# Kernel optimization log

Measured on AMD Instinct MI355X. Metric: run time of the kernel, lower is better.

## Reference

```python
import jax, jax.numpy as jnp
import numpy as np

D_MODEL = 2048
NUM_HEADS = 16
HEAD_DIM = D_MODEL // NUM_HEADS
SCALE = 1.0 / np.sqrt(HEAD_DIM).astype(np.float32)
NEG_INF = -1e9


def setup_inputs() -> dict:
    key = jax.random.key(0)
    ks = jax.random.split(key, 10)
    B, S = 2, 2048
    x = jax.random.normal(ks[0], (B, S, D_MODEL), dtype=jnp.float32)
    # causal lower-triangular mask, broadcastable over (B, H)
    causal_mask = jnp.tril(jnp.ones((S, S), dtype=jnp.int32))[None, None]
    init = 1.0 / np.sqrt(D_MODEL)
    def lin(kw, kb):
        W = jax.random.uniform(kw, (D_MODEL, D_MODEL), jnp.float32, -init, init)
        b = jax.random.uniform(kb, (D_MODEL,), jnp.float32, -init, init)
        return W, b
    Wq, bq = lin(ks[1], ks[2])
    Wk, bk = lin(ks[3], ks[4])
    Wv, bv = lin(ks[5], ks[6])
    Wo, bo = lin(ks[7], ks[8])
    return {"x": x, "causal_mask": causal_mask,
            "Wq": Wq, "bq": bq, "Wk": Wk, "bk": bk,
            "Wv": Wv, "bv": bv, "Wo": Wo, "bo": bo}


def reference(x, causal_mask, Wq, bq, Wk, bk, Wv, bv, Wo, bo):
    B, S, _ = x.shape
    def proj(W, b):
        # torch Linear: x @ W.T + b -> (B, H, S, Dh)
        y = jnp.einsum('bsd,ed->bse', x, W) + b
        return y.reshape(B, S, NUM_HEADS, HEAD_DIM).transpose(0, 2, 1, 3)
    q = proj(Wq, bq)
    k = proj(Wk, bk)
    v = proj(Wv, bv)
    # apply_rope is a no-op stub in the source; q, k unchanged.
    scores = jnp.einsum('bhqd,bhkd->bhqk', q, k) * SCALE
    scores = jnp.where(causal_mask == 0, NEG_INF, scores)
    attn = jax.nn.softmax(scores, axis=-1)
    out = jnp.einsum('bhqk,bhkd->bhqd', attn, v)
    out = out.transpose(0, 2, 1, 3).reshape(B, S, D_MODEL)
    return jnp.einsum('bsd,ed->bse', out, Wo) + bo
```

## Files before the change

kernel.cpp:

```cpp
#include <hip/hip_runtime.h>
#include <hip/hip_bf16.h>
#include <stdint.h>
#include <stddef.h>

typedef __bf16 bf16_t;
typedef __bf16 bf16x4_t __attribute__((ext_vector_type(4)));
typedef __bf16 bf16x8_t __attribute__((ext_vector_type(8)));
typedef float f32x4 __attribute__((ext_vector_type(4)));

#define D_MODEL 2048
#define NHEADS 16
#define HDIM 128
#define SEQ 2048
#define BATCH 2
#define MTOT (BATCH * SEQ)
#define SCALE_F 0.08838834764831845f
#define LOG2E 1.4426950408889634f
#define QSCALE (SCALE_F * LOG2E)
#define KT 64
#define NEGI -3.0e38f
#define MINIT -1.0e30f
#define DEFER_THR 8.0f

#define AS1 __attribute__((address_space(1)))
#define AS3 __attribute__((address_space(3)))

__device__ __forceinline__ void load_lds16(const bf16_t* g, bf16_t* l) {
  __builtin_amdgcn_global_load_lds((AS1 void*)(g), (AS3 void*)(l), 16, 0, 0);
}

__global__ void cast_all_kernel(const float* __restrict__ x,
                                const float* __restrict__ w0, const float* __restrict__ w1,
                                const float* __restrict__ w2, const float* __restrict__ w3,
                                bf16_t* __restrict__ xb, bf16_t* __restrict__ wcat) {
  int i = blockIdx.x * blockDim.x + threadIdx.x;
  const int XN4 = MTOT * D_MODEL / 4;
  const int WN4 = D_MODEL * D_MODEL / 4;
  const float* src;
  bf16_t* dst;
  int idx;
  if (i < XN4) {
    src = x; dst = xb; idx = i;
  } else {
    int j = i - XN4;
    int y = j >> 20;
    idx = j & (WN4 - 1);
    src = (y == 0) ? w0 : (y == 1) ? w1 : (y == 2) ? w2 : w3;
    dst = wcat + (size_t)y * D_MODEL * D_MODEL;
  }
  float4 v = ((const float4*)src)[idx];
  bf16x4_t o;
  o.x = (bf16_t)v.x; o.y = (bf16_t)v.y; o.z = (bf16_t)v.z; o.w = (bf16_t)v.w;
  ((bf16x4_t*)dst)[idx] = o;
}

__global__ __launch_bounds__(256) void gemm_fused(
    const bf16_t* __restrict__ A, const bf16_t* __restrict__ Bm, int mode,
    const float* __restrict__ bias0, const float* __restrict__ bias1,
    const float* __restrict__ bias2,
    bf16_t* __restrict__ Qo, bf16_t* __restrict__ Ko, bf16_t* __restrict__ Vto,
    float* __restrict__ Out) {
  const int K = 2048;
  __shared__ __align__(16) bf16_t lA[128 * 64];
  __shared__ __align__(16) bf16_t lB[128 * 64];
  const int m0 = blockIdx.x * 128;
  const int n0 = blockIdx.y * 128;
  const int t = threadIdx.x;
  const int w = t >> 6, lane = t & 63;
  const int wm = w & 1, wn = w >> 1;
  const int la = lane & 15, lb = lane >> 4;

  f32x4 acc[4][4];
  f32x4 zero = {0.f, 0.f, 0.f, 0.f};
#pragma unroll
  for (int i = 0; i < 4; i++)
#pragma unroll
    for (int j = 0; j < 4; j++) acc[i][j] = zero;

  const int row0 = t >> 3, cc = t & 7;
  const int ccs = cc ^ (row0 & 7);
  const bf16_t* gA = A + (size_t)(m0 + row0) * K + ccs * 8;
  const bf16_t* gB = Bm + (size_t)(n0 + row0) * K + ccs * 8;
  bf16_t* sA = lA + t * 8;
  bf16_t* sB = lB + t * 8;

  for (int k0 = 0; k0 < K; k0 += 64) {
    __syncthreads();
#pragma unroll
    for (int i = 0; i < 4; i++)
      load_lds16(gA + k0 + (size_t)(32 * i) * K, sA + 2048 * i);
#pragma unroll
    for (int i = 0; i < 4; i++)
      load_lds16(gB + k0 + (size_t)(32 * i) * K, sB + 2048 * i);
    __syncthreads();
#pragma unroll
    for (int ks = 0; ks < 2; ks++) {
      bf16x8_t af[4], bfr[4];
#pragma unroll
      for (int mt = 0; mt < 4; mt++) {
        int row = wm * 64 + mt * 16 + la;
        af[mt] = *(const bf16x8_t*)(lA + row * 64 + (((ks * 4 + lb) ^ (la & 7)) * 8));
      }
#pragma unroll
      for (int nt = 0; nt < 4; nt++) {
        int row = wn * 64 + nt * 16 + la;
        bfr[nt] = *(const bf16x8_t*)(lB + row * 64 + (((ks * 4 + lb) ^ (la & 7)) * 8));
      }
#pragma unroll
      for (int mt = 0; mt < 4; mt++)
#pragma unroll
        for (int nt = 0; nt < 4; nt++)
          acc[mt][nt] = __builtin_amdgcn_mfma_f32_16x16x32_bf16(af[mt], bfr[nt], acc[mt][nt], 0, 0, 0);
    }
  }

  if (mode == 0) {
#pragma unroll
    for (int mt = 0; mt < 4; mt++) {
#pragma unroll
      for (int nt = 0; nt < 4; nt++) {
        int m = m0 + wm * 64 + mt * 16 + lb * 4;
        int n = n0 + wn * 64 + nt * 16 + la;
        int b = m >> 11, s = m & 2047;
        int which = n >> 11, hd = n & 2047;
        int h = hd >> 7, d = hd & 127;
        float bv = (which == 0 ? bias0 : which == 1 ? bias1 : bias2)[hd];
        f32x4 v = acc[mt][nt];
        if (which == 2) {
          bf16_t* dst = Vto + ((size_t)(b * NHEADS + h) * HDIM + d) * SEQ + s;
          bf16x4_t pk;
          pk.x = (bf16_t)(v.x + bv); pk.y = (bf16_t)(v.y + bv);
          pk.z = (bf16_t)(v.z + bv); pk.w = (bf16_t)(v.w + bv);
          *(bf16x4_t*)dst = pk;
        } else {
          float sc = (which == 0) ? QSCALE : 1.0f;
          bf16_t* dst = (which == 0 ? Qo : Ko) + ((size_t)(b * NHEADS + h) * SEQ + s) * HDIM + d;
          dst[0]        = (bf16_t)((v.x + bv) * sc);
          dst[HDIM]     = (bf16_t)((v.y + bv) * sc);
          dst[2 * HDIM] = (bf16_t)((v.z + bv) * sc);
          dst[3 * HDIM] = (bf16_t)((v.w + bv) * sc);
        }
      }
    }
  } else {
#pragma unroll
    for (int mt = 0; mt < 4; mt++) {
#pragma unroll
      for (int nt = 0; nt < 4; nt++) {
        int m = m0 + wm * 64 + mt * 16 + lb * 4;
        int n = n0 + wn * 64 + nt * 16 + la;
        float bv = bias0[n];
        f32x4 v = acc[mt][nt];
        float* dst = Out + (size_t)m * D_MODEL + n;
        dst[0]           = v.x + bv;
        dst[D_MODEL]     = v.y + bv;
        dst[2 * D_MODEL] = v.z + bv;
        dst[3 * D_MODEL] = v.w + bv;
      }
    }
  }
}

__global__ __launch_bounds__(256, 2) void flash_attn(
    const bf16_t* __restrict__ Q, const bf16_t* __restrict__ Kg,
    const bf16_t* __restrict__ Vt, bf16_t* __restrict__ O,
    bf16_t* __restrict__ PO, float* __restrict__ ML) {
  __shared__ __align__(16) bf16_t lK[2][KT * 128];
  __shared__ __align__(16) bf16_t lV[128 * KT];
  __shared__ __align__(16) bf16_t lP[128 * 72];
  const int g = blockIdx.x;
  const int bh = g & 31, idx = g >> 5;
  const int t = threadIdx.x;
  const int w = t >> 6, lane = t & 63;
  const int la = lane & 15, lb = lane >> 4;
  const int qloc = w * 32 + la;

  const bf16_t* Qb = Q + (size_t)bh * SEQ * HDIM;
  const bf16_t* Kb = Kg + (size_t)bh * SEQ * HDIM;
  const bf16_t* Vb = Vt + (size_t)bh * HDIM * SEQ;
  const int b = bh >> 4, h = bh & 15;

  int nph, qts[2], k0s[2], k1s[2], slots[2];
  bool parts[2];
  if (idx < 8) {
    nph = 1; qts[0] = 8 + idx; k0s[0] = 0; k1s[0] = 17;
    parts[0] = true; slots[0] = (idx * 32 + bh) * 2;
  } else {
    int qtA = idx - 8;
    nph = 2;
    qts[0] = qtA; k0s[0] = 0; k1s[0] = 2 * qtA + 2; parts[0] = false; slots[0] = 0;
    qts[1] = 15 - qtA; k0s[1] = 17; k1s[1] = 32 - 2 * qtA;
    parts[1] = true; slots[1] = ((7 - qtA) * 32 + bh) * 2 + 1;
  }

  const int krow = t >> 4, kcc = t & 15;
  const int kccx = kcc ^ krow;
  const int vrow = t >> 3, vjc = t & 7;
  const int vccx = vjc ^ (vrow & 7);

  for (int ph = 0; ph < nph; ph++) {
    const int qt = qts[ph], kt0 = k0s[ph], kt1 = k1s[ph];
    const int q0 = qt * 128;

    bf16x8_t qf[2][4];
#pragma unroll
    for (int mt = 0; mt < 2; mt++)
#pragma unroll
      for (int ks = 0; ks < 4; ks++)
        qf[mt][ks] = *(const bf16x8_t*)(Qb + (size_t)(q0 + qloc + mt * 16) * HDIM + ks * 32 + lb * 8);

    f32x4 oacc[2][8];
    float mr[2] = {MINIT, MINIT}, lr[2] = {0.f, 0.f};
    f32x4 zero = {0.f, 0.f, 0.f, 0.f};
#pragma unroll
    for (int mt = 0; mt < 2; mt++)
#pragma unroll
      for (int dt = 0; dt < 8; dt++) oacc[mt][dt] = zero;

    {
      const int j0 = kt0 * KT;
#pragma unroll
      for (int i = 0; i < 4; i++)
        load_lds16(Kb + (size_t)(j0 + krow + 16 * i) * HDIM + kccx * 8,
                   lK[kt0 & 1] + (t + 256 * i) * 8);
    }

    for (int kt = kt0; kt < kt1; kt++) {
      const int j0 = kt * KT;
      const int cur = kt & 1;
      const bool pre = (kt + 1 < kt1);

      __syncthreads();

#pragma unroll
      for (int i = 0; i < 4; i++)
        load_lds16(Vb + (size_t)(vrow + 32 * i) * SEQ + j0 + vccx * 8,
                   lV + (t + 256 * i) * 8);
      if (pre) {
        const int jn = (kt + 1) * KT;
#pragma unroll
        for (int i = 0; i < 4; i++)
          load_lds16(Kb + (size_t)(jn + krow + 16 * i) * HDIM + kccx * 8,
                     lK[cur ^ 1] + (t + 256 * i) * 8);
      }

      f32x4 st[4][2];
#pragma unroll
      for (int nt = 0; nt < 4; nt++)
#pragma unroll
        for (int mt = 0; mt < 2; mt++) st[nt][mt] = zero;
      __builtin_amdgcn_s_setprio(1);
#pragma unroll
      for (int ks = 0; ks < 4; ks++) {
#pragma unroll
        for (int nt = 0; nt < 4; nt++) {
          int j = nt * 16 + la;
          int ck = (ks * 4 + lb) ^ la;
          bf16x8_t kf = *(const bf16x8_t*)(lK[cur] + j * 128 + ck * 8);
#pragma unroll
          for (int mt = 0; mt < 2; mt++)
            st[nt][mt] = __builtin_amdgcn_mfma_f32_16x16x32_bf16(kf, qf[mt][ks], st[nt][mt], 0, 0, 0);
        }
      }
      __builtin_amdgcn_s_setprio(0);

      const bool dm = (j0 + KT > q0);
#pragma unroll
      for (int mt = 0; mt < 2; mt++) {
        int qg = q0 + qloc + mt * 16;
        if (dm) {
#pragma unroll
          for (int nt = 0; nt < 4; nt++)
#pragma unroll
            for (int r = 0; r < 4; r++)
              if (j0 + nt * 16 + lb * 4 + r > qg) st[nt][mt][r] = NEGI;
        }
        float tm = NEGI;
#pragma unroll
        for (int nt = 0; nt < 4; nt++)
#pragma unroll
          for (int r = 0; r < 4; r++) tm = fmaxf(tm, st[nt][mt][r]);
        tm = fmaxf(tm, __shfl_xor(tm, 16));
        tm = fmaxf(tm, __shfl_xor(tm, 32));
        if (!__all(tm - mr[mt] <= DEFER_THR)) {
          float mnew = fmaxf(mr[mt], tm);
          float alpha = exp2f(mr[mt] - mnew);
          lr[mt] *= alpha;
#pragma unroll
          for (int dt = 0; dt < 8; dt++) oacc[mt][dt] *= alpha;
          mr[mt] = mnew;
        }
        float s = 0.f;
#pragma unroll
        for (int nt = 0; nt < 4; nt++) {
          f32x4 p;
#pragma unroll
          for (int r = 0; r < 4; r++) {
            p[r] = exp2f(st[nt][mt][r] - mr[mt]);
            s += p[r];
          }
          bf16x4_t pk;
          pk.x = (bf16_t)p[0]; pk.y = (bf16_t)p[1]; pk.z = (bf16_t)p[2]; pk.w = (bf16_t)p[3];
          *(bf16x4_t*)(lP + (qloc + mt * 16) * 72 + nt * 16 + lb * 4) = pk;
        }
        s += __shfl_xor(s, 16);
        s += __shfl_xor(s, 32);
        lr[mt] += s;
      }

      if (pre) {
        asm volatile("s_waitcnt vmcnt(4)" ::: "memory");
      } else {
        asm volatile("s_waitcnt vmcnt(0)" ::: "memory");
      }
      __builtin_amdgcn_s_barrier();

      bf16x8_t pf[2][2];
#pragma unroll
      for (int mt = 0; mt < 2; mt++)
#pragma unroll
        for (int ksv = 0; ksv < 2; ksv++)
          pf[mt][ksv] = *(const bf16x8_t*)(lP + (w * 32 + mt * 16 + la) * 72 + ksv * 32 + lb * 8);
      __builtin_amdgcn_s_setprio(1);
#pragma unroll
      for (int dt = 0; dt < 8; dt++) {
        int d = dt * 16 + la;
#pragma unroll
        for (int ksv = 0; ksv < 2; ksv++) {
          int jc = (ksv * 4 + lb) ^ (d & 7);
          bf16x8_t vf = *(const bf16x8_t*)(lV + d * 64 + jc * 8);
#pragma unroll
          for (int mt = 0; mt < 2; mt++)
            oacc[mt][dt] = __builtin_amdgcn_mfma_f32_16x16x32_bf16(vf, pf[mt][ksv], oacc[mt][dt], 0, 0, 0);
        }
      }
      __builtin_amdgcn_s_setprio(0);
    }

    if (!parts[ph]) {
#pragma unroll
      for (int mt = 0; mt < 2; mt++) {
        float inv = 1.0f / lr[mt];
        int q = q0 + qloc + mt * 16;
        bf16_t* dst = O + ((size_t)b * SEQ + q) * D_MODEL + h * HDIM + lb * 4;
#pragma unroll
        for (int dt = 0; dt < 8; dt++) {
          f32x4 v = oacc[mt][dt];
          bf16x4_t pk;
          pk.x = (bf16_t)(v[0] * inv); pk.y = (bf16_t)(v[1] * inv);
          pk.z = (bf16_t)(v[2] * inv); pk.w = (bf16_t)(v[3] * inv);
          *(bf16x4_t*)(dst + dt * 16) = pk;
        }
      }
    } else {
      const int slot = slots[ph];
      bf16_t* pob = PO + (size_t)slot * 128 * 128;
#pragma unroll
      for (int mt = 0; mt < 2; mt++) {
        int q = qloc + mt * 16;
        bf16_t* dst = pob + (size_t)q * 128 + lb * 4;
#pragma unroll
        for (int dt = 0; dt < 8; dt++) {
          f32x4 v = oacc[mt][dt];
          bf16x4_t pk;
          pk.x = (bf16_t)v[0]; pk.y = (bf16_t)v[1];
          pk.z = (bf16_t)v[2]; pk.w = (bf16_t)v[3];
          *(bf16x4_t*)(dst + dt * 16) = pk;
        }
        if (lb == 0) {
          float2 ml = make_float2(mr[mt], lr[mt]);
          *(float2*)(ML + ((size_t)slot * 128 + q) * 2) = ml;
        }
      }
    }
  }
}

__global__ void merge_kernel(const bf16_t* __restrict__ PO, const float* __restrict__ ML,
                             bf16_t* __restrict__ O) {
  const int qti = blockIdx.x >> 5, bh = blockIdx.x & 31;
  const int qt = 8 + qti;
  const int t = threadIdx.x;
  const int q = t >> 1, dh = (t & 1) * 64;
  const size_t s1 = ((size_t)(qti * 32 + bh)) * 2;
  const float* ml1 = ML + (s1 * 128 + q) * 2;
  const float* ml2 = ML + ((s1 + 1) * 128 + q) * 2;
  float m1 = ml1[0], l1 = ml1[1], m2 = ml2[0], l2 = ml2[1];
  float m = fmaxf(m1, m2);
  float w1 = exp2f(m1 - m), w2 = exp2f(m2 - m);
  float inv = 1.0f / (w1 * l1 + w2 * l2);
  w1 *= inv; w2 *= inv;
  const bf16_t* p1 = PO + (s1 * 128 + q) * 128 + dh;
  const bf16_t* p2 = PO + ((s1 + 1) * 128 + q) * 128 + dh;
  const int b = bh >> 4, h = bh & 15;
  bf16_t* dst = O + ((size_t)b * SEQ + qt * 128 + q) * D_MODEL + h * HDIM + dh;
#pragma unroll
  for (int i = 0; i < 8; i++) {
    bf16x8_t a = ((const bf16x8_t*)p1)[i];
    bf16x8_t c = ((const bf16x8_t*)p2)[i];
    bf16x8_t o;
#pragma unroll
    for (int e = 0; e < 8; e++)
      o[e] = (bf16_t)(w1 * (float)a[e] + w2 * (float)c[e]);
    ((bf16x8_t*)dst)[i] = o;
  }
}

extern "C" void kernel_launch(void* const* d_in, const int* in_sizes, int n_in,
                              void* d_out, int out_size, void* d_ws, size_t ws_size,
                              hipStream_t stream) {
  (void)in_sizes; (void)n_in; (void)out_size; (void)ws_size;
  const float* x  = (const float*)d_in[0];
  const float* Wq = (const float*)d_in[2];
  const float* bq = (const float*)d_in[3];
  const float* Wk = (const float*)d_in[4];
  const float* bk = (const float*)d_in[5];
  const float* Wv = (const float*)d_in[6];
  const float* bv = (const float*)d_in[7];
  const float* Wo = (const float*)d_in[8];
  const float* bo = (const float*)d_in[9];
  float* out = (float*)d_out;

  const size_t NBF = (size_t)MTOT * D_MODEL * sizeof(bf16_t);
  const size_t WBF = (size_t)D_MODEL * D_MODEL * sizeof(bf16_t);
  char* p = (char*)d_ws;
  bf16_t* xb   = (bf16_t*)p; p += NBF;
  bf16_t* Wcat = (bf16_t*)p; p += 4 * WBF;
  bf16_t* Qb   = (bf16_t*)p; p += NBF;
  bf16_t* Kb   = (bf16_t*)p; p += NBF;
  bf16_t* Vtb  = (bf16_t*)p; p += NBF;
  bf16_t* Wob  = Wcat + (size_t)3 * D_MODEL * D_MODEL;
  bf16_t* Ob   = xb;
  bf16_t* PO = Wcat;
  float*  ML = (float*)(Wcat + (size_t)512 * 128 * 128);

  const int XN4 = MTOT * D_MODEL / 4;
  const int WN4 = D_MODEL * D_MODEL / 4;
  cast_all_kernel<<<(XN4 + 4 * WN4) / 256, 256, 0, stream>>>(x, Wq, Wk, Wv, Wo, xb, Wcat);

  gemm_fused<<<dim3(MTOT / 128, 6144 / 128), 256, 0, stream>>>(
      xb, Wcat, 0, bq, bk, bv, Qb, Kb, Vtb, nullptr);

  flash_attn<<<dim3(512), 256, 0, stream>>>(Qb, Kb, Vtb, Ob, PO, ML);
  merge_kernel<<<dim3(256), 256, 0, stream>>>(PO, ML, Ob);

  gemm_fused<<<dim3(MTOT / 128, D_MODEL / 128), 256, 0, stream>>>(
      Ob, Wob, 1, bo, nullptr, nullptr, nullptr, nullptr, nullptr, out);
}
```

Before: 376.7 us.

## Add 256x256-tile double-buffered QKV GEMM with phased LDS staging

Replaces the 128x128 QKV projection GEMM with a new 256x256-tile kernel using 512 threads, double-buffered LDS, and an 8-phase schedule that interleaves async global-to-LDS staging of the next K slice with MFMA compute, using setprio and fine-grained vmcnt waits. Larger tiles raise arithmetic intensity and cut global traffic. The pipelining is meant to hide load latency behind MFMA work. The cost is 128 KB of LDS per block and high register use, which limits occupancy, and the grid shrinks to 16x24=384 blocks, which may leave some CUs underused.

```diff
diff --git a/kernel.cpp b/kernel.cpp
--- a/kernel.cpp
+++ b/kernel.cpp
@@ -52,6 +52,146 @@
   bf16x4_t o;
   o.x = (bf16_t)v.x; o.y = (bf16_t)v.y; o.z = (bf16_t)v.z; o.w = (bf16_t)v.w;
   ((bf16x4_t*)dst)[idx] = o;
+}
+
+__global__ __launch_bounds__(512, 2) void gemm256_qkv(
+    const bf16_t* __restrict__ A, const bf16_t* __restrict__ Bm,
+    const float* __restrict__ bias0, const float* __restrict__ bias1,
+    const float* __restrict__ bias2,
+    bf16_t* __restrict__ Qo, bf16_t* __restrict__ Ko, bf16_t* __restrict__ Vto) {
+  const int K = 2048;
+  __shared__ __align__(16) bf16_t lA[2][256 * 64];
+  __shared__ __align__(16) bf16_t lB[2][256 * 64];
+  const int m0 = blockIdx.x * 256;
+  const int n0 = blockIdx.y * 256;
+  const int t = threadIdx.x;
+  const int w = t >> 6, lane = t & 63;
+  const int wm = w & 1, wn = w >> 1;
+  const int la = lane & 15, lb = lane >> 4;
+
+  f32x4 acc[8][4];
+  f32x4 zero = {0.f, 0.f, 0.f, 0.f};
+#pragma unroll
+  for (int i = 0; i < 8; i++)
+#pragma unroll
+    for (int j = 0; j < 4; j++) acc[i][j] = zero;
+
+  const int srow = t >> 3, cc = t & 7;
+  const int ccs = cc ^ (srow & 7);
+  const bf16_t* gA0 = A + (size_t)m0 * K + ccs * 8;
+  const bf16_t* gB0 = Bm + (size_t)n0 * K + ccs * 8;
+
+  auto stageHalfA = [&](int buf, int h, int k0) {
+#pragma unroll
+    for (int i = 0; i < 2; i++) {
+      int row = h * 128 + srow + 64 * i;
+      load_lds16(gA0 + k0 + (size_t)row * K, &lA[buf][0] + row * 64 + cc * 8);
+    }
+  };
+  auto stageHalfB = [&](int buf, int h, int k0) {
+#pragma unroll
+    for (int i = 0; i < 2; i++) {
+      int row = h * 128 + srow + 64 * i;
+      load_lds16(gB0 + k0 + (size_t)row * K, &lB[buf][0] + row * 64 + cc * 8);
+    }
+  };
+
+  bf16x8_t bfr[4][2];
+  bf16x8_t af[2][2];
+  auto loadBf = [&](int buf) {
+#pragma unroll
+    for (int nt = 0; nt < 4; nt++)
+#pragma unroll
+      for (int ks = 0; ks < 2; ks++) {
+        int row = wn * 64 + nt * 16 + la;
+        bfr[nt][ks] = *(const bf16x8_t*)(&lB[buf][0] + row * 64 + (((ks * 4 + lb) ^ (la & 7)) * 8));
+      }
+  };
+  auto loadAf = [&](int buf, int mt0) {
+#pragma unroll
+    for (int q = 0; q < 2; q++)
+#pragma unroll
+      for (int ks = 0; ks < 2; ks++) {
+        int row = wm * 128 + (mt0 + q) * 16 + la;
+        af[q][ks] = *(const bf16x8_t*)(&lA[buf][0] + row * 64 + (((ks * 4 + lb) ^ (la & 7)) * 8));
+      }
+  };
+  auto mfma16 = [&](int mt0) {
+#pragma unroll
+    for (int ks = 0; ks < 2; ks++)
+#pragma unroll
+      for (int q = 0; q < 2; q++)
+#pragma unroll
+        for (int nt = 0; nt < 4; nt++)
+          acc[mt0 + q][nt] =
+              __builtin_amdgcn_mfma_f32_16x16x32_bf16(af[q][ks], bfr[nt][ks], acc[mt0 + q][nt], 0, 0, 0);
+  };
+
+  auto phase = [&](int buf, int mt0, bool ldB, int stageOp, int sBuf, int sH, int sK0, int vm) {
+    if (ldB) loadBf(buf);
+    loadAf(buf, mt0);
+    if (stageOp == 1) stageHalfA(sBuf, sH, sK0);
+    else if (stageOp == 2) stageHalfB(sBuf, sH, sK0);
+    __builtin_amdgcn_s_barrier();
+    asm volatile("s_waitcnt lgkmcnt(0)" ::: "memory");
+    __builtin_amdgcn_s_setprio(1);
+    mfma16(mt0);
+    __builtin_amdgcn_s_setprio(0);
+    if (vm == 4) asm volatile("s_waitcnt vmcnt(4)" ::: "memory");
+    else if (vm == 0) asm volatile("s_waitcnt vmcnt(0)" ::: "memory");
+    __builtin_amdgcn_s_barrier();
+  };
+
+  stageHalfB(0, 0, 0); stageHalfB(0, 1, 0);
+  stageHalfA(0, 0, 0); stageHalfA(0, 1, 0);
+  stageHalfB(1, 0, 64); stageHalfB(1, 1, 64);
+  asm volatile("s_waitcnt vmcnt(4)" ::: "memory");
+  __builtin_amdgcn_s_barrier();
+
+  for (int it = 0; it < 16; it++) {
+    const int T1 = 2 * it + 1;
+    const bool pre = (it < 15);
+    const int k1 = T1 * 64;
+    const int k2 = (2 * it + 2) * 64;
+    const int k3 = (2 * it + 3) * 64;
+
+    phase(0, 0, true,  1, 1, 0, k1, -1);
+    phase(0, 2, false, 1, 1, 1, k1, -1);
+    phase(0, 4, false, pre ? 2 : 0, 0, 0, k2, -1);
+    phase(0, 6, false, pre ? 2 : 0, 0, 1, k2, pre ? 4 : 0);
+    phase(1, 0, true,  pre ? 1 : 0, 0, 0, k2, -1);
+    phase(1, 2, false, pre ? 1 : 0, 0, 1, k2, -1);
+    phase(1, 4, false, pre ? 2 : 0, 1, 0, k3, -1);
+    phase(1, 6, false, pre ? 2 : 0, 1, 1, k3, 4);
+  }
+
+#pragma unroll
+  for (int mt = 0; mt < 8; mt++) {
+#pragma unroll
+    for (int nt = 0; nt < 4; nt++) {
+      int m = m0 + wm * 128 + mt * 16 + lb * 4;
+      int n = n0 + wn * 64 + nt * 16 + la;
+      int bb = m >> 11, s = m & 2047;
+      int which = n >> 11, hd = n & 2047;
+      int h = hd >> 7, d = hd & 127;
+      float bv = (which == 0 ? bias0 : which == 1 ? bias1 : bias2)[hd];
+      f32x4 v = acc[mt][nt];
+      if (which == 2) {
+        bf16_t* dst = Vto + ((size_t)(bb * NHEADS + h) * HDIM + d) * SEQ + s;
+        bf16x4_t pk;
+        pk.x = (bf16_t)(v.x + bv); pk.y = (bf16_t)(v.y + bv);
+        pk.z = (bf16_t)(v.z + bv); pk.w = (bf16_t)(v.w + bv);
+        *(bf16x4_t*)dst = pk;
+      } else {
+        float sc = (which == 0) ? QSCALE : 1.0f;
+        bf16_t* dst = (which == 0 ? Qo : Ko) + ((size_t)(bb * NHEADS + h) * SEQ + s) * HDIM + d;
+        dst[0]        = (bf16_t)((v.x + bv) * sc);
+        dst[HDIM]     = (bf16_t)((v.y + bv) * sc);
+        dst[2 * HDIM] = (bf16_t)((v.z + bv) * sc);
+        dst[3 * HDIM] = (bf16_t)((v.w + bv) * sc);
+      }
+    }
+  }
 }
 
 __global__ __launch_bounds__(256) void gemm_fused(
@@ -438,8 +578,8 @@
   const int WN4 = D_MODEL * D_MODEL / 4;
   cast_all_kernel<<<(XN4 + 4 * WN4) / 256, 256, 0, stream>>>(x, Wq, Wk, Wv, Wo, xb, Wcat);
 
-  gemm_fused<<<dim3(MTOT / 128, 6144 / 128), 256, 0, stream>>>(
-      xb, Wcat, 0, bq, bk, bv, Qb, Kb, Vtb, nullptr);
+  gemm256_qkv<<<dim3(MTOT / 256, 6144 / 256), 512, 0, stream>>>(
+      xb, Wcat, bq, bk, bv, Qb, Kb, Vtb);
 
   flash_attn<<<dim3(512), 256, 0, stream>>>(Qb, Kb, Vtb, Ob, PO, ML);
   merge_kernel<<<dim3(256), 256, 0, stream>>>(PO, ML, Ob);
```

Measured after the change: 392.2 us. 4.1% more time.
